# Kernel optimization log

Hardware: AMD Instinct MI355X
Metric: run time of the kernel (lower is better)

## Reference

```python
import jax, jax.numpy as jnp
import numpy as np


def Qmat(V):
    """Chain of Householder reflections: Q = I @ H(v_0) @ ... @ H(v_{d-1}).

    Faithful to the source: columns of V are normalized, H(v) = I - 2 v v^T.
    M @ H(v) == M - 2 (M v) v^T, so each step is a matvec + rank-1 update
    (same math as the source's full GEMM, O(d^2) per step instead of O(d^3)).
    """
    d = V.shape[0]
    # torch.norm(V.T, 2, dim=1) == L2 norm of each column of V
    norms = jnp.linalg.norm(V, axis=0)  # (d,)
    Vn = V / norms[None, :]

    def step(M, v):
        Mv = M @ v                        # (d,)
        return M - 2.0 * jnp.outer(Mv, v), None

    M0 = jnp.eye(d, dtype=V.dtype)
    M, _ = jax.lax.scan(step, M0, Vn.T)   # iterate over columns v_i
    return M


def setup_inputs() -> dict:
    key = jax.random.key(0)
    k1, k2 = jax.random.split(key)
    ci, co = 1024, 2048
    U = 0.05 * jax.random.normal(k1, (ci, ci), dtype=jnp.float32)
    V = 0.05 * jax.random.normal(k2, (co, co), dtype=jnp.float32)
    return {"U": U, "V": V}


def reference(U, V):
    ci, co = U.shape[0], V.shape[0]
    Qu = Qmat(U)  # (ci, ci) orthogonal
    Qv = Qmat(V)  # (co, co) orthogonal
    if ci < co:
        weight = Qu @ Qv[:ci, :]      # (ci, co)
    else:
        weight = Qu[:, :co] @ Qv      # (ci, co)
    return weight
```

## Files before the change

### kernel.cpp

```cpp
#include <hip/hip_runtime.h>
#include <hip/hip_bf16.h>
#include <cstdint>

#define CI 1024
#define CO 2048
#define LP 36

typedef float  fx4  __attribute__((ext_vector_type(4)));
typedef short  s16x4 __attribute__((ext_vector_type(4)));
typedef short  s16x8 __attribute__((ext_vector_type(8)));
typedef unsigned short u16;

#define MFMA(a,b,c) __builtin_amdgcn_mfma_f32_16x16x32_bf16((a),(b),(c),0,0,0)

__device__ __forceinline__ u16 f2b(float x) {
    __hip_bfloat16 h = __float2bfloat16(x);
    return __builtin_bit_cast(u16, h);
}
__device__ __forceinline__ float b2f(u16 u) {
    __hip_bfloat16 h = __builtin_bit_cast(__hip_bfloat16, u);
    return __bfloat162float(h);
}


__global__ __launch_bounds__(256) void colnorm2(const float* __restrict__ M, float* __restrict__ n2, int d) {
    int c = blockIdx.x * 256 + threadIdx.x;
    int r0 = blockIdx.y * 64;
    float s = 0.0f;
    for (int r = r0; r < r0 + 64; ++r) {
        float v = M[(size_t)r * d + c];
        s = fmaf(v, v, s);
    }
    atomicAdd(&n2[c], s);
}

__global__ __launch_bounds__(256) void trans_planes_n(const float* __restrict__ X, int d,
                                                      const float* __restrict__ n2,
                                                      u16* __restrict__ Th, u16* __restrict__ Tl) {
    __shared__ float tile[32][33];
    int t = threadIdx.x;
    int r = t >> 3, c4 = (t & 7) * 4;
    int bx = blockIdx.x, by = blockIdx.y;
    fx4 v = *(const fx4*)(X + (size_t)(by * 32 + r) * d + bx * 32 + c4);
    tile[r][c4 + 0] = v[0]; tile[r][c4 + 1] = v[1]; tile[r][c4 + 2] = v[2]; tile[r][c4 + 3] = v[3];
    __syncthreads();
    int a = bx * 32 + r;
    float sc = 1.0f / sqrtf(n2[a]);
    u16 h[4], l[4];
    #pragma unroll
    for (int j = 0; j < 4; ++j) {
        float f = tile[c4 + j][r] * sc;
        u16 hb = f2b(f);
        h[j] = hb;
        l[j] = f2b(f - b2f(hb));
    }
    size_t o = (size_t)a * d + by * 32 + c4;
    *(s16x4*)&Th[o] = *(s16x4*)&h[0];
    *(s16x4*)&Tl[o] = *(s16x4*)&l[0];
}

__global__ __launch_bounds__(256) void planes_n(const float* __restrict__ X, int d,
                                                const float* __restrict__ n2,
                                                u16* __restrict__ Ph, u16* __restrict__ Pl) {
    size_t idx = ((size_t)blockIdx.x * 256 + threadIdx.x) * 8;
    int c = (int)(idx & (size_t)(d - 1));
    fx4 v0 = *(const fx4*)(X + idx);
    fx4 v1 = *(const fx4*)(X + idx + 4);
    u16 h[8], l[8];
    #pragma unroll
    for (int j = 0; j < 8; ++j) {
        float f = ((j < 4) ? v0[j] : v1[j - 4]) * (1.0f / sqrtf(n2[c + j]));
        u16 hb = f2b(f);
        h[j] = hb;
        l[j] = f2b(f - b2f(hb));
    }
    *(s16x4*)&Ph[idx]     = *(s16x4*)&h[0];
    *(s16x4*)&Ph[idx + 4] = *(s16x4*)&h[4];
    *(s16x4*)&Pl[idx]     = *(s16x4*)&l[0];
    *(s16x4*)&Pl[idx + 4] = *(s16x4*)&l[4];
}

__global__ __launch_bounds__(256) void planes_conv(const float* __restrict__ X,
                                                   u16* __restrict__ Ph, u16* __restrict__ Pl) {
    size_t idx = ((size_t)blockIdx.x * 256 + threadIdx.x) * 8;
    fx4 v0 = *(const fx4*)(X + idx);
    fx4 v1 = *(const fx4*)(X + idx + 4);
    u16 h[8], l[8];
    #pragma unroll
    for (int j = 0; j < 8; ++j) {
        float f = (j < 4) ? v0[j] : v1[j - 4];
        u16 hb = f2b(f);
        h[j] = hb;
        l[j] = f2b(f - b2f(hb));
    }
    *(s16x4*)&Ph[idx]     = *(s16x4*)&h[0];
    *(s16x4*)&Ph[idx + 4] = *(s16x4*)&h[4];
    *(s16x4*)&Pl[idx]     = *(s16x4*)&l[0];
    *(s16x4*)&Pl[idx + 4] = *(s16x4*)&l[4];
}

__device__ __forceinline__ void mma_step(const u16 Ah[][LP], const u16 Al[][LP],
                                         const u16 Bh[][LP], const u16 Bl[][LP],
                                         int wr, int wc, int lane, fx4 acc[2][2]) {
    int kb = (lane >> 4) * 8;
    int rl = lane & 15;
    s16x8 ah[2], al[2], bh[2], bl[2];
    #pragma unroll
    for (int f = 0; f < 2; ++f) {
        int ra = wr * 32 + f * 16 + rl;
        s16x4 p = *(const s16x4*)&Ah[ra][kb];
        s16x4 q = *(const s16x4*)&Ah[ra][kb + 4];
        ah[f] = __builtin_shufflevector(p, q, 0,1,2,3,4,5,6,7);
        p = *(const s16x4*)&Al[ra][kb];
        q = *(const s16x4*)&Al[ra][kb + 4];
        al[f] = __builtin_shufflevector(p, q, 0,1,2,3,4,5,6,7);
        int rb = wc * 32 + f * 16 + rl;
        p = *(const s16x4*)&Bh[rb][kb];
        q = *(const s16x4*)&Bh[rb][kb + 4];
        bh[f] = __builtin_shufflevector(p, q, 0,1,2,3,4,5,6,7);
        p = *(const s16x4*)&Bl[rb][kb];
        q = *(const s16x4*)&Bl[rb][kb + 4];
        bl[f] = __builtin_shufflevector(p, q, 0,1,2,3,4,5,6,7);
    }
    #pragma unroll
    for (int i = 0; i < 2; ++i)
        #pragma unroll
        for (int j = 0; j < 2; ++j) {
            acc[i][j] = MFMA(ah[i], bh[j], acc[i][j]);
            acc[i][j] = MFMA(ah[i], bl[j], acc[i][j]);
            acc[i][j] = MFMA(al[i], bh[j], acc[i][j]);
        }
}

__device__ __forceinline__ void stage_f32(const float* __restrict__ A, int ldA,
                                          int m0, int k0, int t, u16 Dh[][LP], u16 Dl[][LP]) {
    int row = t >> 2, kc = (t & 3) * 8;
    const float* p = A + (size_t)(m0 + row) * ldA + k0 + kc;
    fx4 v0 = *(const fx4*)p;
    fx4 v1 = *(const fx4*)(p + 4);
    u16 h[8], l[8];
    #pragma unroll
    for (int j = 0; j < 8; ++j) {
        float f = (j < 4) ? v0[j] : v1[j - 4];
        u16 hb = f2b(f);
        h[j] = hb;
        l[j] = f2b(f - b2f(hb));
    }
    *(s16x4*)&Dh[row][kc]     = *(s16x4*)&h[0];
    *(s16x4*)&Dh[row][kc + 4] = *(s16x4*)&h[4];
    *(s16x4*)&Dl[row][kc]     = *(s16x4*)&l[0];
    *(s16x4*)&Dl[row][kc + 4] = *(s16x4*)&l[4];
}

__device__ __forceinline__ void stage_planes(const u16* __restrict__ Ph, const u16* __restrict__ Pl, int ld,
                                             int n0, int k0, int t, u16 Dh[][LP], u16 Dl[][LP]) {
    int row = t >> 2, kc = (t & 3) * 8;
    size_t o = (size_t)(n0 + row) * ld + k0 + kc;
    *(s16x4*)&Dh[row][kc]     = *(const s16x4*)(Ph + o);
    *(s16x4*)&Dh[row][kc + 4] = *(const s16x4*)(Ph + o + 4);
    *(s16x4*)&Dl[row][kc]     = *(const s16x4*)(Pl + o);
    *(s16x4*)&Dl[row][kc + 4] = *(const s16x4*)(Pl + o + 4);
}

struct GJob {
    const u16* Ph; const u16* Pl; int ld;
    int a, b;
    float* out; int ldO;
};

__device__ __forceinline__ GJob gdecode(int t,
                                        const u16* Uh, const u16* Ul, const u16* Vh, const u16* Vl,
                                        float* Sd, float* Nt64, float* Nt128, float* Nt256, float* Nt512) {
    GJob g;
    if (t < 48) {
        bool isU = t < 16; int off = 64 * (isU ? t : t - 16);
        g.Ph = isU ? Uh : Vh; g.Pl = isU ? Ul : Vl; g.ld = isU ? CI : CO;
        g.a = off; g.b = off;
        g.out = Sd + (size_t)t * 4096; g.ldO = 64;
    } else if (t < 72) {
        int j = t - 48; bool isU = j < 8; int p = isU ? j : j - 8;
        int c0 = 128 * p, r1 = c0 + 64;
        g.Ph = isU ? Uh : Vh; g.Pl = isU ? Ul : Vl; g.ld = isU ? CI : CO;
        g.a = r1; g.b = c0;
        g.out = Nt64 + (size_t)j * 4096; g.ldO = 64;
    } else if (t < 120) {
        int j = t - 72; int pair = j >> 2, q = j & 3, my = q >> 1, mx = q & 1;
        bool isU = pair < 4; int p = isU ? pair : pair - 4;
        int c0 = 256 * p, r1 = c0 + 128;
        g.Ph = isU ? Uh : Vh; g.Pl = isU ? Ul : Vl; g.ld = isU ? CI : CO;
        g.a = r1 + 64 * my; g.b = c0 + 64 * mx;
        g.out = Nt128 + (size_t)pair * 16384 + (size_t)(64 * my) * 128 + 64 * mx; g.ldO = 128;
    } else if (t < 216) {
        int j = t - 120; int pair = j >> 4, q = j & 15, my = q >> 2, mx = q & 3;
        bool isU = pair < 2; int p = isU ? pair : pair - 2;
        int c0 = 512 * p, r1 = c0 + 256;
        g.Ph = isU ? Uh : Vh; g.Pl = isU ? Ul : Vl; g.ld = isU ? CI : CO;
        g.a = r1 + 64 * my; g.b = c0 + 64 * mx;
        g.out = Nt256 + (size_t)pair * 65536 + (size_t)(64 * my) * 256 + 64 * mx; g.ldO = 256;
    } else {
        int j = t - 216; int pair = j >> 6, q = j & 63, my = q >> 3, mx = q & 7;
        int c0 = 1024 * pair, r1 = c0 + 512;
        g.Ph = Vh; g.Pl = Vl; g.ld = CO;
        g.a = r1 + 64 * my; g.b = c0 + 64 * mx;
        g.out = Nt512 + (size_t)pair * 262144 + (size_t)(64 * my) * 512 + 64 * mx; g.ldO = 512;
    }
    return g;
}

__global__ __launch_bounds__(256) void gram_nt_sk(const u16* __restrict__ Uh, const u16* __restrict__ Ul,
                                                  const u16* __restrict__ Vh, const u16* __restrict__ Vl,
                                                  float* Sd, float* Nt64, float* Nt128, float* Nt256, float* Nt512,
                                                  float* __restrict__ Gp) {
    int tt = blockIdx.x, ks = blockIdx.y;
    GJob g = gdecode(tt, Uh, Ul, Vh, Vl, Sd, Nt64, Nt128, Nt256, Nt512);
    int kchunk = g.ld >> 3;
    int kb = ks * kchunk;
    float* C = Gp + ((size_t)tt * 8 + ks) * 4096;
    __shared__ u16 Ah[64][LP], Al[64][LP], Bh_[64][LP], Bl_[64][LP];
    int t = threadIdx.x, lane = t & 63, w = t >> 6, wr = w >> 1, wc = w & 1;
    fx4 acc[2][2] = {};
    for (int k0 = kb; k0 < kb + kchunk; k0 += 32) {
        stage_planes(g.Ph, g.Pl, g.ld, g.a, k0, t, Ah, Al);
        stage_planes(g.Ph, g.Pl, g.ld, g.b, k0, t, Bh_, Bl_);
        __syncthreads();
        mma_step(Ah, Al, Bh_, Bl_, wr, wc, lane, acc);
        __syncthreads();
    }
    #pragma unroll
    for (int fr = 0; fr < 2; ++fr)
        #pragma unroll
        for (int fc = 0; fc < 2; ++fc) {
            int row = wr * 32 + fr * 16 + ((lane >> 4) << 2);
            int col = wc * 32 + fc * 16 + (lane & 15);
            #pragma unroll
            for (int r = 0; r < 4; ++r)
                C[(size_t)(row + r) * 64 + col] = acc[fr][fc][r];
        }
}

__global__ __launch_bounds__(256) void gcombine(const float* __restrict__ Gp,
                                                const u16* Uh, const u16* Ul, const u16* Vh, const u16* Vl,
                                                float* Sd, float* Nt64, float* Nt128, float* Nt256, float* Nt512) {
    int tt = blockIdx.x;
    GJob g = gdecode(tt, Uh, Ul, Vh, Vl, Sd, Nt64, Nt128, Nt256, Nt512);
    const float* base = Gp + (size_t)tt * 8 * 4096;
    for (int i = threadIdx.x; i < 4096; i += 256) {
        float s = 0.0f;
        #pragma unroll
        for (int ks = 0; ks < 8; ++ks) s += base[(size_t)ks * 4096 + i];
        g.out[(size_t)(i >> 6) * g.ldO + (i & 63)] = s;
    }
}

__global__ __launch_bounds__(64) void diag_inv64(const float* __restrict__ Sd,
                                                 float* __restrict__ Ttu, float* __restrict__ Ttv) {
    int j = blockIdx.x;
    int y = blockIdx.y;
    const float* S = Sd + (size_t)y * 4096;
    float* T; int ldT, off;
    if (y < 16) { T = Ttu; ldT = CI; off = 64 * y; }
    else        { T = Ttv; ldT = CO; off = 64 * (y - 16); }
    float* Trow = T + (size_t)(off + j) * ldT + off;
    int l = threadIdx.x;
    float x = (l == j) ? 2.0f : 0.0f;
    float a = 0.0f;
    int jpad = (j + 7) & ~7;
    float q0=0,q1=0,q2=0,q3=0,q4=0,q5=0,q6=0,q7=0;
#define LR(Q, R) { int _r = (R); if (_r >= 1 && _r <= j) Q = S[(size_t)_r * 64 + l]; }
    LR(q0, jpad - 0) LR(q1, jpad - 1) LR(q2, jpad - 2) LR(q3, jpad - 3)
    LR(q4, jpad - 4) LR(q5, jpad - 5) LR(q6, jpad - 6) LR(q7, jpad - 7)
#define ST(Q) { \
    float yk = __shfl(x, k); \
    a = fmaf(Q, yk, a); \
    if (k <= j && l == k - 1) x = -2.0f * a; \
    int pr = k - 8; \
    if (pr >= 1) Q = S[(size_t)pr * 64 + l]; \
    --k; }
    int k = jpad;
    int ng = jpad >> 3;
    for (int g = 0; g < ng; ++g) {
        ST(q0) ST(q1) ST(q2) ST(q3) ST(q4) ST(q5) ST(q6) ST(q7)
    }
#undef ST
#undef LR
    Trow[l] = x;
}

__global__ __launch_bounds__(256) void merge64_fused(const float* __restrict__ Nt64,
                                                     float* __restrict__ Ttu, float* __restrict__ Ttv) {
    int p = blockIdx.x;
    bool isU = p < 8;
    float* Tt = isU ? Ttu : Ttv;
    int ldT = isU ? CI : CO;
    int pp = isU ? p : p - 8;
    int c0 = 128 * pp, r1 = c0 + 64;
    __shared__ float A[64][65], B[64][65], Tm[64][65];
    int t = threadIdx.x;
    int r = t >> 2, c = (t & 3) * 16;
    #pragma unroll
    for (int j = 0; j < 16; ++j) A[r][c + j] = Nt64[(size_t)p * 4096 + (size_t)r * 64 + c + j];
    #pragma unroll
    for (int j = 0; j < 16; ++j) B[r][c + j] = Tt[(size_t)(c0 + r) * ldT + c0 + c + j];
    __syncthreads();
    float acc[16];
    #pragma unroll
    for (int j = 0; j < 16; ++j) acc[j] = 0.0f;
    for (int k = 0; k < 64; ++k) {
        float av = A[r][k];
        #pragma unroll
        for (int j = 0; j < 16; ++j) acc[j] = fmaf(av, B[k][c + j], acc[j]);
    }
    __syncthreads();
    #pragma unroll
    for (int j = 0; j < 16; ++j) Tm[r][c + j] = acc[j];
    #pragma unroll
    for (int j = 0; j < 16; ++j) A[r][c + j] = Tt[(size_t)(r1 + r) * ldT + r1 + c + j];
    __syncthreads();
    #pragma unroll
    for (int j = 0; j < 16; ++j) acc[j] = 0.0f;
    for (int k = 0; k < 64; ++k) {
        float av = A[r][k];
        #pragma unroll
        for (int j = 0; j < 16; ++j) acc[j] = fmaf(av, Tm[k][c + j], acc[j]);
    }
    #pragma unroll
    for (int j = 0; j < 16; ++j)
        Tt[(size_t)(r1 + r) * ldT + c0 + c + j] = -acc[j];
}

__device__ __forceinline__ void fgemm_sk_body(const float* __restrict__ A, int lda,
                                              const float* __restrict__ B, int ldb,
                                              float* __restrict__ P, int kb, int klen) {
    int m0 = blockIdx.y * 64, n0 = blockIdx.x * 64;
    __shared__ float As[16][64];
    __shared__ float Bs[16][64];
    int tid = threadIdx.x;
    int tm = (tid >> 4) * 8, tn = (tid & 15) * 4;
    int ar = tid >> 2, ac = (tid & 3) * 4;
    int bk = tid >> 4, bn = (tid & 15) * 4;
    float acc[8][4] = {};
    for (int k0 = kb; k0 < kb + klen; k0 += 16) {
        #pragma unroll
        for (int p = 0; p < 2; ++p) {
            int r = ar + p * 32;
            fx4 av = *(const fx4*)(A + (size_t)(m0 + r) * lda + k0 + ac);
            As[ac + 0][r] = av[0]; As[ac + 1][r] = av[1]; As[ac + 2][r] = av[2]; As[ac + 3][r] = av[3];
        }
        #pragma unroll
        for (int p = 0; p < 2; ++p) {
            int kk = bk + p * 8;
            *(fx4*)&Bs[kk][bn] = *(const fx4*)(B + (size_t)(k0 + kk) * ldb + n0 + bn);
        }
        __syncthreads();
        #pragma unroll
        for (int k = 0; k < 16; ++k) {
            fx4 alo = *(const fx4*)&As[k][tm];
            fx4 ahi = *(const fx4*)&As[k][tm + 4];
            fx4 bv  = *(const fx4*)&Bs[k][tn];
            float aa[8] = {alo[0], alo[1], alo[2], alo[3], ahi[0], ahi[1], ahi[2], ahi[3]};
            float bb[4] = {bv[0], bv[1], bv[2], bv[3]};
            #pragma unroll
            for (int i = 0; i < 8; ++i)
                #pragma unroll
                for (int jj = 0; jj < 4; ++jj) acc[i][jj] = fmaf(aa[i], bb[jj], acc[i][jj]);
        }
        __syncthreads();
    }
    #pragma unroll
    for (int i = 0; i < 8; ++i) {
        fx4 v = { acc[i][0], acc[i][1], acc[i][2], acc[i][3] };
        *(fx4*)(P + (size_t)(tm + i) * 64 + tn) = v;
    }
}

__global__ __launch_bounds__(128) void merge_a_sk(const float* __restrict__ NtL, int s, int KS,
                                                  const float* __restrict__ Ttu, const float* __restrict__ Ttv,
                                                  int npu, float* __restrict__ Mp) {
    int z = blockIdx.z;
    int pair = z / KS, ks = z % KS;
    const float* Tt; int ldT, p;
    if (pair < npu) { Tt = Ttu; ldT = CI; p = pair; } else { Tt = Ttv; ldT = CO; p = pair - npu; }
    int c0 = 2 * s * p;
    int gx = s >> 6;
    int tile = (pair * gx + blockIdx.y) * gx + blockIdx.x;
    int klen = s / KS;
    fgemm_sk_body(NtL + (size_t)pair * s * s, s, Tt + (size_t)c0 * ldT + c0, ldT,
                  Mp + ((size_t)tile * KS + ks) * 4096, ks * klen, klen);
}

__global__ __launch_bounds__(128) void merge_b_sk(const float* __restrict__ tmp, int s, int KS,
                                                  const float* __restrict__ Ttu, const float* __restrict__ Ttv,
                                                  int npu, float* __restrict__ Mp) {
    int z = blockIdx.z;
    int pair = z / KS, ks = z % KS;
    const float* Tt; int ldT, p;
    if (pair < npu) { Tt = Ttu; ldT = CI; p = pair; } else { Tt = Ttv; ldT = CO; p = pair - npu; }
    int c0 = 2 * s * p, r1 = c0 + s;
    int gx = s >> 6;
    int tile = (pair * gx + blockIdx.y) * gx + blockIdx.x;
    int klen = s / KS;
    fgemm_sk_body(Tt + (size_t)r1 * ldT + r1, ldT, tmp + (size_t)pair * s * s, s,
                  Mp + ((size_t)tile * KS + ks) * 4096, ks * klen, klen);
}

__global__ __launch_bounds__(256) void macomb(const float* __restrict__ Mp, int KS, int s,
                                              float* __restrict__ tmp) {
    int tile = blockIdx.x;
    int gx = s >> 6, per = gx * gx;
    int pair = tile / per, rem = tile % per, by = rem / gx, bx = rem % gx;
    float* dst = tmp + (size_t)pair * s * s + (size_t)(by * 64) * s + bx * 64;
    const float* base = Mp + (size_t)tile * KS * 4096;
    for (int i = threadIdx.x; i < 4096; i += 256) {
        float v = 0.0f;
        for (int k = 0; k < KS; ++k) v += base[(size_t)k * 4096 + i];
        dst[(size_t)(i >> 6) * s + (i & 63)] = v;
    }
}

__global__ __launch_bounds__(256) void mbcomb(const float* __restrict__ Mp, int KS, int s, int npu,
                                              float* __restrict__ Ttu, float* __restrict__ Ttv) {
    int tile = blockIdx.x;
    int gx = s >> 6, per = gx * gx;
    int pair = tile / per, rem = tile % per, by = rem / gx, bx = rem % gx;
    float* Tt; int ldT, p;
    if (pair < npu) { Tt = Ttu; ldT = CI; p = pair; } else { Tt = Ttv; ldT = CO; p = pair - npu; }
    int c0 = 2 * s * p, r1 = c0 + s;
    float* dst = Tt + (size_t)(r1 + by * 64) * ldT + c0 + bx * 64;
    const float* base = Mp + (size_t)tile * KS * 4096;
    for (int i = threadIdx.x; i < 4096; i += 256) {
        float v = 0.0f;
        for (int k = 0; k < KS; ++k) v += base[(size_t)k * 4096 + i];
        dst[(size_t)(i >> 6) * ldT + (i & 63)] = -v;
    }
}

__global__ __launch_bounds__(256) void gemm_pp_sk(const u16* __restrict__ Ah_, const u16* __restrict__ Al_, int ldA,
                                                  const u16* __restrict__ Bh0, const u16* __restrict__ Bl0, int ldB,
                                                  float* __restrict__ Pp, int kchunk) {
    int N = gridDim.x * 64;
    size_t MN = (size_t)gridDim.x * gridDim.y * 4096;
    float* C = Pp + (size_t)blockIdx.z * MN;
    int kb = blockIdx.z * kchunk;
    __shared__ u16 Ah[64][LP], Al[64][LP], Bh_[64][LP], Bl_[64][LP];
    int t = threadIdx.x, lane = t & 63, w = t >> 6, wr = w >> 1, wc = w & 1;
    int m0 = blockIdx.y * 64, n0 = blockIdx.x * 64;
    fx4 acc[2][2] = {};
    for (int k0 = kb; k0 < kb + kchunk; k0 += 32) {
        stage_planes(Ah_, Al_, ldA, m0, k0, t, Ah, Al);
        stage_planes(Bh0, Bl0, ldB, n0, k0, t, Bh_, Bl_);
        __syncthreads();
        mma_step(Ah, Al, Bh_, Bl_, wr, wc, lane, acc);
        __syncthreads();
    }
    #pragma unroll
    for (int fr = 0; fr < 2; ++fr)
        #pragma unroll
        for (int fc = 0; fc < 2; ++fc) {
            int row = m0 + wr * 32 + fr * 16 + ((lane >> 4) << 2);
            int col = n0 + wc * 32 + fc * 16 + (lane & 15);
            #pragma unroll
            for (int r = 0; r < 4; ++r)
                C[(size_t)(row + r) * N + col] = acc[fr][fc][r];
        }
}

__global__ __launch_bounds__(256) void gemm_fp_sk(const float* __restrict__ A, int ldA,
                                                  const u16* __restrict__ Bh0, const u16* __restrict__ Bl0, int ldB,
                                                  float* __restrict__ Pp, int kchunk) {
    int N = gridDim.x * 64;
    size_t MN = (size_t)gridDim.x * gridDim.y * 4096;
    float* C = Pp + (size_t)blockIdx.z * MN;
    int kb = blockIdx.z * kchunk;
    __shared__ u16 Ah[64][LP], Al[64][LP], Bh_[64][LP], Bl_[64][LP];
    int t = threadIdx.x, lane = t & 63, w = t >> 6, wr = w >> 1, wc = w & 1;
    int m0 = blockIdx.y * 64, n0 = blockIdx.x * 64;
    fx4 acc[2][2] = {};
    for (int k0 = kb; k0 < kb + kchunk; k0 += 32) {
        stage_f32(A, ldA, m0, k0, t, Ah, Al);
        stage_planes(Bh0, Bl0, ldB, n0, k0, t, Bh_, Bl_);
        __syncthreads();
        mma_step(Ah, Al, Bh_, Bl_, wr, wc, lane, acc);
        __syncthreads();
    }
    #pragma unroll
    for (int fr = 0; fr < 2; ++fr)
        #pragma unroll
        for (int fc = 0; fc < 2; ++fc) {
            int row = m0 + wr * 32 + fr * 16 + ((lane >> 4) << 2);
            int col = n0 + wc * 32 + fc * 16 + (lane & 15);
            #pragma unroll
            for (int r = 0; r < 4; ++r)
                C[(size_t)(row + r) * N + col] = acc[fr][fc][r];
        }
}

template<int MODE>
__global__ __launch_bounds__(256) void combine(const float* __restrict__ Pp, int S,
                                               const float* __restrict__ aux, int ldaux,
                                               float* __restrict__ C, int N) {
    size_t MN = (size_t)gridDim.x * 2048;
    int gid = blockIdx.x * 256 + threadIdx.x;
    size_t idx = (size_t)gid * 8;
    int nv = N >> 3;
    int row = gid / nv, col = (gid % nv) * 8;
    fx4 s0 = *(const fx4*)(Pp + idx);
    fx4 s1 = *(const fx4*)(Pp + idx + 4);
    for (int s = 1; s < S; ++s) {
        const float* p = Pp + (size_t)s * MN + idx;
        s0 += *(const fx4*)p;
        s1 += *(const fx4*)(p + 4);
    }
    float out[8];
    #pragma unroll
    for (int j = 0; j < 8; ++j) {
        float a = (j < 4) ? s0[j] : s1[j - 4];
        if (MODE == 0)      out[j] = a;
        else if (MODE == 1) out[j] = ((col + j) == row ? 1.0f : 0.0f) - a;
        else if (MODE == 2) out[j] = aux[(size_t)row * ldaux + col + j] - a;
        else if (MODE == 3) out[j] = C[(size_t)row * N + col + j] - a;
        else                out[j] = ((col + j) < CI ? aux[(size_t)row * ldaux + col + j] : 0.0f) - a;
    }
    *(fx4*)(C + (size_t)row * N + col)     = *(fx4*)&out[0];
    *(fx4*)(C + (size_t)row * N + col + 4) = *(fx4*)&out[4];
}

extern "C" void kernel_launch(void* const* d_in, const int* in_sizes, int n_in,
                              void* d_out, int out_size, void* d_ws, size_t ws_size,
                              hipStream_t stream) {
    const float* U = (const float*)d_in[0];
    const float* V = (const float*)d_in[1];
    float* W = (float*)d_out;

    char* ws = (char*)d_ws;
    u16*   Unth = (u16*)  (ws + ((size_t)0   << 20));
    u16*   Untl = (u16*)  (ws + ((size_t)2   << 20));
    u16*   Unh  = (u16*)  (ws + ((size_t)4   << 20));
    u16*   Unl  = (u16*)  (ws + ((size_t)6   << 20));
    u16*   Vnth = (u16*)  (ws + ((size_t)8   << 20));
    u16*   Vntl = (u16*)  (ws + ((size_t)16  << 20));
    u16*   Vnh  = (u16*)  (ws + ((size_t)24  << 20));
    u16*   Vnl  = (u16*)  (ws + ((size_t)32  << 20));
    float* Ttu  = (float*)(ws + ((size_t)40  << 20));
    float* Ttv  = (float*)(ws + ((size_t)44  << 20));
    u16*   Mtuh = (u16*)  (ws + ((size_t)60  << 20));
    u16*   Mtul = (u16*)  (ws + ((size_t)62  << 20));
    u16*   Mtvh = (u16*)  (ws + ((size_t)64  << 20));
    u16*   Mtvl = (u16*)  (ws + ((size_t)72  << 20));
    float* Sd   = (float*)(ws + ((size_t)80  << 20));
    float* NtA  = (float*)(ws + ((size_t)81  << 20));
    float* tmp  = (float*)(ws + ((size_t)86  << 20));
    float* X1   = (float*)(ws + ((size_t)88  << 20));
    float* Qp   = (float*)(ws + ((size_t)90  << 20));
    float* H1u  = (float*)(ws + ((size_t)94  << 20));
    float* H2u  = (float*)(ws + ((size_t)96  << 20));
    float* Qu   = (float*)(ws + ((size_t)98  << 20));
    float* H1   = (float*)(ws + ((size_t)102 << 20));
    float* H2   = (float*)(ws + ((size_t)106 << 20));
    float* H3   = (float*)(ws + ((size_t)110 << 20));
    float* H4   = (float*)(ws + ((size_t)114 << 20));
    float* n2u  = (float*)(ws + ((size_t)118 << 20));
    float* n2v  = n2u + CI;
    float* Pp   = (float*)(ws + ((size_t)120 << 20));
    float* Gp   = (float*)(ws + ((size_t)120 << 20));
    float* Mp   = Gp;

    float* Nt64  = NtA;
    float* Nt128 = NtA + 98304;
    float* Nt256 = NtA + 294912;
    float* Nt512 = NtA + 688128;

    hipMemsetAsync(n2u, 0, (CI + CO) * sizeof(float), stream);
    colnorm2<<<dim3(CI / 256, CI / 64), dim3(256), 0, stream>>>(U, n2u, CI);
    colnorm2<<<dim3(CO / 256, CO / 64), dim3(256), 0, stream>>>(V, n2v, CO);

    trans_planes_n<<<dim3(CI / 32, CI / 32), dim3(256), 0, stream>>>(U, CI, n2u, Unth, Untl);
    trans_planes_n<<<dim3(CO / 32, CO / 32), dim3(256), 0, stream>>>(V, CO, n2v, Vnth, Vntl);
    planes_n<<<dim3(CI * CI / 2048), dim3(256), 0, stream>>>(U, CI, n2u, Unh, Unl);
    planes_n<<<dim3(CO * CO / 2048), dim3(256), 0, stream>>>(V, CO, n2v, Vnh, Vnl);

    gram_nt_sk<<<dim3(344, 8), dim3(256), 0, stream>>>(Unth, Untl, Vnth, Vntl,
                                                       Sd, Nt64, Nt128, Nt256, Nt512, Gp);
    gcombine<<<dim3(344), dim3(256), 0, stream>>>(Gp, Unth, Untl, Vnth, Vntl,
                                                  Sd, Nt64, Nt128, Nt256, Nt512);

    hipMemsetAsync(Ttu, 0, (size_t)20 << 20, stream);
    diag_inv64<<<dim3(64, 48), dim3(64), 0, stream>>>(Sd, Ttu, Ttv);
    merge64_fused<<<dim3(24), dim3(256), 0, stream>>>(Nt64, Ttu, Ttv);
    merge_a_sk<<<dim3(2, 2, 48), dim3(128), 0, stream>>>(Nt128, 128, 4, Ttu, Ttv, 4, Mp);
    macomb<<<dim3(48), dim3(256), 0, stream>>>(Mp, 4, 128, tmp);
    merge_b_sk<<<dim3(2, 2, 48), dim3(128), 0, stream>>>(tmp, 128, 4, Ttu, Ttv, 4, Mp);
    mbcomb<<<dim3(48), dim3(256), 0, stream>>>(Mp, 4, 128, 4, Ttu, Ttv);
    merge_a_sk<<<dim3(4, 4, 24), dim3(128), 0, stream>>>(Nt256, 256, 4, Ttu, Ttv, 2, Mp);
    macomb<<<dim3(96), dim3(256), 0, stream>>>(Mp, 4, 256, tmp);
    merge_b_sk<<<dim3(4, 4, 24), dim3(128), 0, stream>>>(tmp, 256, 4, Ttu, Ttv, 2, Mp);
    mbcomb<<<dim3(96), dim3(256), 0, stream>>>(Mp, 4, 256, 2, Ttu, Ttv);
    merge_a_sk<<<dim3(8, 8, 16), dim3(128), 0, stream>>>(Nt512, 512, 8, Ttu, Ttv, 0, Mp);
    macomb<<<dim3(128), dim3(256), 0, stream>>>(Mp, 8, 512, tmp);
    merge_b_sk<<<dim3(8, 8, 16), dim3(128), 0, stream>>>(tmp, 512, 8, Ttu, Ttv, 0, Mp);
    mbcomb<<<dim3(128), dim3(256), 0, stream>>>(Mp, 8, 512, 0, Ttu, Ttv);

    planes_conv<<<dim3(CI * CI / 2048), dim3(256), 0, stream>>>(Ttu, Mtuh, Mtul);
    planes_conv<<<dim3(CO * CO / 2048), dim3(256), 0, stream>>>(Ttv, Mtvh, Mtvl);

    gemm_pp_sk<<<dim3(8, 16, 4), dim3(256), 0, stream>>>(Unh, Unl, CI, Mtuh, Mtul, CI, Pp, 128);
    combine<0><<<dim3(CI * 512 / 2048), dim3(256), 0, stream>>>(Pp, 4, nullptr, 0, X1, 512);
    gemm_fp_sk<<<dim3(16, 16, 4), dim3(256), 0, stream>>>(X1, 512, Unh, Unl, CI, Pp, 128);
    combine<1><<<dim3(CI * CI / 2048), dim3(256), 0, stream>>>(Pp, 4, nullptr, 0, Qp, CI);
    gemm_fp_sk<<<dim3(8, 16, 4), dim3(256), 0, stream>>>(Qp, CI, Unth + (size_t)512 * CI, Untl + (size_t)512 * CI, CI, Pp, 256);
    combine<0><<<dim3(CI * 512 / 2048), dim3(256), 0, stream>>>(Pp, 4, nullptr, 0, H1u, 512);
    gemm_fp_sk<<<dim3(8, 16, 4), dim3(256), 0, stream>>>(H1u, 512, Mtuh + (size_t)512 * CI + 512,
                                                         Mtul + (size_t)512 * CI + 512, CI, Pp, 128);
    combine<0><<<dim3(CI * 512 / 2048), dim3(256), 0, stream>>>(Pp, 4, nullptr, 0, H2u, 512);
    gemm_fp_sk<<<dim3(16, 16, 4), dim3(256), 0, stream>>>(H2u, 512, Unh + 512, Unl + 512, CI, Pp, 128);
    combine<2><<<dim3(CI * CI / 2048), dim3(256), 0, stream>>>(Pp, 4, Qp, CI, Qu, CI);

    gemm_fp_sk<<<dim3(16, 16, 4), dim3(256), 0, stream>>>(Qu, CI, Vnth, Vntl, CO, Pp, 256);
    combine<0><<<dim3(CI * CI / 2048), dim3(256), 0, stream>>>(Pp, 4, nullptr, 0, H1, CI);
    gemm_fp_sk<<<dim3(16, 16, 4), dim3(256), 0, stream>>>(H1, CI, Mtvh, Mtvl, CO, Pp, 256);
    combine<0><<<dim3(CI * CI / 2048), dim3(256), 0, stream>>>(Pp, 4, nullptr, 0, H2, CI);
    gemm_fp_sk<<<dim3(32, 16, 2), dim3(256), 0, stream>>>(H2, CI, Vnh, Vnl, CO, Pp, 512);
    combine<4><<<dim3(CI * CO / 2048), dim3(256), 0, stream>>>(Pp, 2, Qu, CI, W, CO);
    gemm_fp_sk<<<dim3(16, 16, 4), dim3(256), 0, stream>>>(W, CO, Vnth + (size_t)1024 * CO, Vntl + (size_t)1024 * CO, CO, Pp, 512);
    combine<0><<<dim3(CI * CI / 2048), dim3(256), 0, stream>>>(Pp, 4, nullptr, 0, H3, CI);
    gemm_fp_sk<<<dim3(16, 16, 4), dim3(256), 0, stream>>>(H3, CI, Mtvh + (size_t)1024 * CO + 1024,
                                                          Mtvl + (size_t)1024 * CO + 1024, CO, Pp, 256);
    combine<0><<<dim3(CI * CI / 2048), dim3(256), 0, stream>>>(Pp, 4, nullptr, 0, H4, CI);
    gemm_fp_sk<<<dim3(32, 16, 2), dim3(256), 0, stream>>>(H4, CI, Vnh + 1024, Vnl + 1024, CO, Pp, 512);
    combine<3><<<dim3(CI * CO / 2048), dim3(256), 0, stream>>>(Pp, 2, nullptr, 0, W, CO);
}
```

Before: 504.9 us.

## Double-buffer LDS tiles with register prefetch in the split-K GEMM kernels

Three split-K GEMM kernels (gram, plane-plane, f32-plane) now load the next k-tile into registers while MFMAs run on the current LDS buffer, then commit it to the other half of a double-buffered shared array. This removes one __syncthreads per iteration and hides global load latency behind compute. For diagonal Gram tiles (a==b) the B tile is not loaded again and A is reused as B. The cost is twice the LDS footprint and more registers, which may lower occupancy.

```diff
diff --git a/kernel.cpp b/kernel.cpp
--- a/kernel.cpp
+++ b/kernel.cpp
@@ -132,34 +132,48 @@
         }
 }
 
-__device__ __forceinline__ void stage_f32(const float* __restrict__ A, int ldA,
-                                          int m0, int k0, int t, u16 Dh[][LP], u16 Dl[][LP]) {
+struct PF { s16x4 a, b, c, d; };
+__device__ __forceinline__ PF fetch_pl(const u16* __restrict__ Ph, const u16* __restrict__ Pl, int ld,
+                                       int n0, int k0, int t) {
+    int row = t >> 2, kc = (t & 3) * 8;
+    size_t o = (size_t)(n0 + row) * ld + k0 + kc;
+    PF f;
+    f.a = *(const s16x4*)(Ph + o);
+    f.b = *(const s16x4*)(Ph + o + 4);
+    f.c = *(const s16x4*)(Pl + o);
+    f.d = *(const s16x4*)(Pl + o + 4);
+    return f;
+}
+__device__ __forceinline__ void commit_pl(const PF& f, u16 Dh[][LP], u16 Dl[][LP], int t) {
+    int row = t >> 2, kc = (t & 3) * 8;
+    *(s16x4*)&Dh[row][kc]     = f.a;
+    *(s16x4*)&Dh[row][kc + 4] = f.b;
+    *(s16x4*)&Dl[row][kc]     = f.c;
+    *(s16x4*)&Dl[row][kc + 4] = f.d;
+}
+struct FF { fx4 v0, v1; };
+__device__ __forceinline__ FF fetch_f32(const float* __restrict__ A, int ldA, int m0, int k0, int t) {
     int row = t >> 2, kc = (t & 3) * 8;
     const float* p = A + (size_t)(m0 + row) * ldA + k0 + kc;
-    fx4 v0 = *(const fx4*)p;
-    fx4 v1 = *(const fx4*)(p + 4);
+    FF f;
+    f.v0 = *(const fx4*)p;
+    f.v1 = *(const fx4*)(p + 4);
+    return f;
+}
+__device__ __forceinline__ void commit_f32(const FF& f, u16 Dh[][LP], u16 Dl[][LP], int t) {
+    int row = t >> 2, kc = (t & 3) * 8;
     u16 h[8], l[8];
     #pragma unroll
     for (int j = 0; j < 8; ++j) {
-        float f = (j < 4) ? v0[j] : v1[j - 4];
-        u16 hb = f2b(f);
+        float v = (j < 4) ? f.v0[j] : f.v1[j - 4];
+        u16 hb = f2b(v);
         h[j] = hb;
-        l[j] = f2b(f - b2f(hb));
+        l[j] = f2b(v - b2f(hb));
     }
     *(s16x4*)&Dh[row][kc]     = *(s16x4*)&h[0];
     *(s16x4*)&Dh[row][kc + 4] = *(s16x4*)&h[4];
     *(s16x4*)&Dl[row][kc]     = *(s16x4*)&l[0];
     *(s16x4*)&Dl[row][kc + 4] = *(s16x4*)&l[4];
-}
-
-__device__ __forceinline__ void stage_planes(const u16* __restrict__ Ph, const u16* __restrict__ Pl, int ld,
-                                             int n0, int k0, int t, u16 Dh[][LP], u16 Dl[][LP]) {
-    int row = t >> 2, kc = (t & 3) * 8;
-    size_t o = (size_t)(n0 + row) * ld + k0 + kc;
-    *(s16x4*)&Dh[row][kc]     = *(const s16x4*)(Ph + o);
-    *(s16x4*)&Dh[row][kc + 4] = *(const s16x4*)(Ph + o + 4);
-    *(s16x4*)&Dl[row][kc]     = *(const s16x4*)(Pl + o);
-    *(s16x4*)&Dl[row][kc + 4] = *(const s16x4*)(Pl + o + 4);
 }
 
 struct GJob {
@@ -213,18 +227,34 @@
                                                   float* __restrict__ Gp) {
     int tt = blockIdx.x, ks = blockIdx.y;
     GJob g = gdecode(tt, Uh, Ul, Vh, Vl, Sd, Nt64, Nt128, Nt256, Nt512);
+    bool same = (g.a == g.b);
     int kchunk = g.ld >> 3;
     int kb = ks * kchunk;
     float* C = Gp + ((size_t)tt * 8 + ks) * 4096;
-    __shared__ u16 Ah[64][LP], Al[64][LP], Bh_[64][LP], Bl_[64][LP];
+    __shared__ u16 Ah[2][64][LP], Al[2][64][LP], Bh_[2][64][LP], Bl_[2][64][LP];
     int t = threadIdx.x, lane = t & 63, w = t >> 6, wr = w >> 1, wc = w & 1;
     fx4 acc[2][2] = {};
-    for (int k0 = kb; k0 < kb + kchunk; k0 += 32) {
-        stage_planes(g.Ph, g.Pl, g.ld, g.a, k0, t, Ah, Al);
-        stage_planes(g.Ph, g.Pl, g.ld, g.b, k0, t, Bh_, Bl_);
-        __syncthreads();
-        mma_step(Ah, Al, Bh_, Bl_, wr, wc, lane, acc);
-        __syncthreads();
+    PF fa = fetch_pl(g.Ph, g.Pl, g.ld, g.a, kb, t);
+    PF fb;
+    if (!same) fb = fetch_pl(g.Ph, g.Pl, g.ld, g.b, kb, t);
+    commit_pl(fa, Ah[0], Al[0], t);
+    if (!same) commit_pl(fb, Bh_[0], Bl_[0], t);
+    __syncthreads();
+    int nt = kchunk >> 5;
+    for (int it = 0; it < nt; ++it) {
+        int cur = it & 1;
+        if (it + 1 < nt) {
+            int k0 = kb + (it + 1) * 32;
+            fa = fetch_pl(g.Ph, g.Pl, g.ld, g.a, k0, t);
+            if (!same) fb = fetch_pl(g.Ph, g.Pl, g.ld, g.b, k0, t);
+        }
+        mma_step(Ah[cur], Al[cur], same ? Ah[cur] : Bh_[cur], same ? Al[cur] : Bl_[cur], wr, wc, lane, acc);
+        if (it + 1 < nt) {
+            int nx = cur ^ 1;
+            commit_pl(fa, Ah[nx], Al[nx], t);
+            if (!same) commit_pl(fb, Bh_[nx], Bl_[nx], t);
+            __syncthreads();
+        }
     }
     #pragma unroll
     for (int fr = 0; fr < 2; ++fr)
@@ -441,16 +471,30 @@
     size_t MN = (size_t)gridDim.x * gridDim.y * 4096;
     float* C = Pp + (size_t)blockIdx.z * MN;
     int kb = blockIdx.z * kchunk;
-    __shared__ u16 Ah[64][LP], Al[64][LP], Bh_[64][LP], Bl_[64][LP];
+    __shared__ u16 Ah[2][64][LP], Al[2][64][LP], Bh_[2][64][LP], Bl_[2][64][LP];
     int t = threadIdx.x, lane = t & 63, w = t >> 6, wr = w >> 1, wc = w & 1;
     int m0 = blockIdx.y * 64, n0 = blockIdx.x * 64;
     fx4 acc[2][2] = {};
-    for (int k0 = kb; k0 < kb + kchunk; k0 += 32) {
-        stage_planes(Ah_, Al_, ldA, m0, k0, t, Ah, Al);
-        stage_planes(Bh0, Bl0, ldB, n0, k0, t, Bh_, Bl_);
-        __syncthreads();
-        mma_step(Ah, Al, Bh_, Bl_, wr, wc, lane, acc);
-        __syncthreads();
+    PF fa = fetch_pl(Ah_, Al_, ldA, m0, kb, t);
+    PF fb = fetch_pl(Bh0, Bl0, ldB, n0, kb, t);
+    commit_pl(fa, Ah[0], Al[0], t);
+    commit_pl(fb, Bh_[0], Bl_[0], t);
+    __syncthreads();
+    int nt = kchunk >> 5;
+    for (int it = 0; it < nt; ++it) {
+        int cur = it & 1;
+        if (it + 1 < nt) {
+            int k0 = kb + (it + 1) * 32;
+            fa = fetch_pl(Ah_, Al_, ldA, m0, k0, t);
+            fb = fetch_pl(Bh0, Bl0, ldB, n0, k0, t);
+        }
+        mma_step(Ah[cur], Al[cur], Bh_[cur], Bl_[cur], wr, wc, lane, acc);
+        if (it + 1 < nt) {
+            int nx = cur ^ 1;
+            commit_pl(fa, Ah[nx], Al[nx], t);
+            commit_pl(fb, Bh_[nx], Bl_[nx], t);
+            __syncthreads();
+        }
     }
     #pragma unroll
     for (int fr = 0; fr < 2; ++fr)
@@ -471,16 +515,30 @@
     size_t MN = (size_t)gridDim.x * gridDim.y * 4096;
     float* C = Pp + (size_t)blockIdx.z * MN;
     int kb = blockIdx.z * kchunk;
-    __shared__ u16 Ah[64][LP], Al[64][LP], Bh_[64][LP], Bl_[64][LP];
+    __shared__ u16 Ah[2][64][LP], Al[2][64][LP], Bh_[2][64][LP], Bl_[2][64][LP];
     int t = threadIdx.x, lane = t & 63, w = t >> 6, wr = w >> 1, wc = w & 1;
     int m0 = blockIdx.y * 64, n0 = blockIdx.x * 64;
     fx4 acc[2][2] = {};
-    for (int k0 = kb; k0 < kb + kchunk; k0 += 32) {
-        stage_f32(A, ldA, m0, k0, t, Ah, Al);
-        stage_planes(Bh0, Bl0, ldB, n0, k0, t, Bh_, Bl_);
-        __syncthreads();
-        mma_step(Ah, Al, Bh_, Bl_, wr, wc, lane, acc);
-        __syncthreads();
+    FF fa = fetch_f32(A, ldA, m0, kb, t);
+    PF fb = fetch_pl(Bh0, Bl0, ldB, n0, kb, t);
+    commit_f32(fa, Ah[0], Al[0], t);
+    commit_pl(fb, Bh_[0], Bl_[0], t);
+    __syncthreads();
+    int nt = kchunk >> 5;
+    for (int it = 0; it < nt; ++it) {
+        int cur = it & 1;
+        if (it + 1 < nt) {
+            int k0 = kb + (it + 1) * 32;
+            fa = fetch_f32(A, ldA, m0, k0, t);
+            fb = fetch_pl(Bh0, Bl0, ldB, n0, k0, t);
+        }
+        mma_step(Ah[cur], Al[cur], Bh_[cur], Bl_[cur], wr, wc, lane, acc);
+        if (it + 1 < nt) {
+            int nx = cur ^ 1;
+            commit_f32(fa, Ah[nx], Al[nx], t);
+            commit_pl(fb, Bh_[nx], Bl_[nx], t);
+            __syncthreads();
+        }
     }
     #pragma unroll
     for (int fr = 0; fr < 2; ++fr)
```

Result: no change. 500.3 us (median of 2 runs) (-0.9%).

## Emit bf16 hi/lo planes from combine and prefetch GEMM tiles into registers

Applied to the files above, without the earlier changes.

The combine kernels now write bf16 hi/lo split planes directly, and fp32 only where a later step still needs it. That lets every downstream GEMM use the plane-input kernel instead of re-splitting fp32 operands inside each tile load, and it removes the fp32 intermediate buffers. The GEMM and Gram loops now prefetch the next k-tile into registers while the MFMAs run on the current shared-memory tile. The Gram kernel also skips loading B when it is identical to A. The LDS row pitch grows to 40 so that 16-byte vector LDS loads stay aligned, at the cost of slightly more shared memory and extra register pressure from the prefetch.

```diff
diff --git a/kernel.cpp b/kernel.cpp
--- a/kernel.cpp
+++ b/kernel.cpp
@@ -4,7 +4,7 @@
 
 #define CI 1024
 #define CO 2048
-#define LP 36
+#define LP 40
 
 typedef float  fx4  __attribute__((ext_vector_type(4)));
 typedef short  s16x4 __attribute__((ext_vector_type(4)));
@@ -108,19 +108,11 @@
     #pragma unroll
     for (int f = 0; f < 2; ++f) {
         int ra = wr * 32 + f * 16 + rl;
-        s16x4 p = *(const s16x4*)&Ah[ra][kb];
-        s16x4 q = *(const s16x4*)&Ah[ra][kb + 4];
-        ah[f] = __builtin_shufflevector(p, q, 0,1,2,3,4,5,6,7);
-        p = *(const s16x4*)&Al[ra][kb];
-        q = *(const s16x4*)&Al[ra][kb + 4];
-        al[f] = __builtin_shufflevector(p, q, 0,1,2,3,4,5,6,7);
+        ah[f] = *(const s16x8*)&Ah[ra][kb];
+        al[f] = *(const s16x8*)&Al[ra][kb];
         int rb = wc * 32 + f * 16 + rl;
-        p = *(const s16x4*)&Bh[rb][kb];
-        q = *(const s16x4*)&Bh[rb][kb + 4];
-        bh[f] = __builtin_shufflevector(p, q, 0,1,2,3,4,5,6,7);
-        p = *(const s16x4*)&Bl[rb][kb];
-        q = *(const s16x4*)&Bl[rb][kb + 4];
-        bl[f] = __builtin_shufflevector(p, q, 0,1,2,3,4,5,6,7);
+        bh[f] = *(const s16x8*)&Bh[rb][kb];
+        bl[f] = *(const s16x8*)&Bl[rb][kb];
     }
     #pragma unroll
     for (int i = 0; i < 2; ++i)
@@ -132,34 +124,20 @@
         }
 }
 
-__device__ __forceinline__ void stage_f32(const float* __restrict__ A, int ldA,
-                                          int m0, int k0, int t, u16 Dh[][LP], u16 Dl[][LP]) {
-    int row = t >> 2, kc = (t & 3) * 8;
-    const float* p = A + (size_t)(m0 + row) * ldA + k0 + kc;
-    fx4 v0 = *(const fx4*)p;
-    fx4 v1 = *(const fx4*)(p + 4);
-    u16 h[8], l[8];
-    #pragma unroll
-    for (int j = 0; j < 8; ++j) {
-        float f = (j < 4) ? v0[j] : v1[j - 4];
-        u16 hb = f2b(f);
-        h[j] = hb;
-        l[j] = f2b(f - b2f(hb));
-    }
-    *(s16x4*)&Dh[row][kc]     = *(s16x4*)&h[0];
-    *(s16x4*)&Dh[row][kc + 4] = *(s16x4*)&h[4];
-    *(s16x4*)&Dl[row][kc]     = *(s16x4*)&l[0];
-    *(s16x4*)&Dl[row][kc + 4] = *(s16x4*)&l[4];
-}
-
-__device__ __forceinline__ void stage_planes(const u16* __restrict__ Ph, const u16* __restrict__ Pl, int ld,
-                                             int n0, int k0, int t, u16 Dh[][LP], u16 Dl[][LP]) {
+struct PF { s16x8 h, l; };
+__device__ __forceinline__ PF fetch_pl(const u16* __restrict__ Ph, const u16* __restrict__ Pl, int ld,
+                                       int n0, int k0, int t) {
     int row = t >> 2, kc = (t & 3) * 8;
     size_t o = (size_t)(n0 + row) * ld + k0 + kc;
-    *(s16x4*)&Dh[row][kc]     = *(const s16x4*)(Ph + o);
-    *(s16x4*)&Dh[row][kc + 4] = *(const s16x4*)(Ph + o + 4);
-    *(s16x4*)&Dl[row][kc]     = *(const s16x4*)(Pl + o);
-    *(s16x4*)&Dl[row][kc + 4] = *(const s16x4*)(Pl + o + 4);
+    PF f;
+    f.h = *(const s16x8*)(Ph + o);
+    f.l = *(const s16x8*)(Pl + o);
+    return f;
+}
+__device__ __forceinline__ void commit_pl(const PF& f, u16 Dh[][LP], u16 Dl[][LP], int t) {
+    int row = t >> 2, kc = (t & 3) * 8;
+    *(s16x8*)&Dh[row][kc] = f.h;
+    *(s16x8*)&Dl[row][kc] = f.l;
 }
 
 struct GJob {
@@ -213,17 +191,27 @@
                                                   float* __restrict__ Gp) {
     int tt = blockIdx.x, ks = blockIdx.y;
     GJob g = gdecode(tt, Uh, Ul, Vh, Vl, Sd, Nt64, Nt128, Nt256, Nt512);
+    bool same = (g.a == g.b);
     int kchunk = g.ld >> 3;
     int kb = ks * kchunk;
     float* C = Gp + ((size_t)tt * 8 + ks) * 4096;
     __shared__ u16 Ah[64][LP], Al[64][LP], Bh_[64][LP], Bl_[64][LP];
     int t = threadIdx.x, lane = t & 63, w = t >> 6, wr = w >> 1, wc = w & 1;
     fx4 acc[2][2] = {};
-    for (int k0 = kb; k0 < kb + kchunk; k0 += 32) {
-        stage_planes(g.Ph, g.Pl, g.ld, g.a, k0, t, Ah, Al);
-        stage_planes(g.Ph, g.Pl, g.ld, g.b, k0, t, Bh_, Bl_);
+    PF fa = fetch_pl(g.Ph, g.Pl, g.ld, g.a, kb, t);
+    PF fb;
+    if (!same) fb = fetch_pl(g.Ph, g.Pl, g.ld, g.b, kb, t);
+    int nt = kchunk >> 5;
+    for (int it = 0; it < nt; ++it) {
+        commit_pl(fa, Ah, Al, t);
+        if (!same) commit_pl(fb, Bh_, Bl_, t);
         __syncthreads();
-        mma_step(Ah, Al, Bh_, Bl_, wr, wc, lane, acc);
+        if (it + 1 < nt) {
+            int k0 = kb + (it + 1) * 32;
+            fa = fetch_pl(g.Ph, g.Pl, g.ld, g.a, k0, t);
+            if (!same) fb = fetch_pl(g.Ph, g.Pl, g.ld, g.b, k0, t);
+        }
+        mma_step(Ah, Al, same ? Ah : Bh_, same ? Al : Bl_, wr, wc, lane, acc);
         __syncthreads();
     }
     #pragma unroll
@@ -445,10 +433,18 @@
     int t = threadIdx.x, lane = t & 63, w = t >> 6, wr = w >> 1, wc = w & 1;
     int m0 = blockIdx.y * 64, n0 = blockIdx.x * 64;
     fx4 acc[2][2] = {};
-    for (int k0 = kb; k0 < kb + kchunk; k0 += 32) {
-        stage_planes(Ah_, Al_, ldA, m0, k0, t, Ah, Al);
-        stage_planes(Bh0, Bl0, ldB, n0, k0, t, Bh_, Bl_);
+    PF fa = fetch_pl(Ah_, Al_, ldA, m0, kb, t);
+    PF fb = fetch_pl(Bh0, Bl0, ldB, n0, kb, t);
+    int nt = kchunk >> 5;
+    for (int it = 0; it < nt; ++it) {
+        commit_pl(fa, Ah, Al, t);
+        commit_pl(fb, Bh_, Bl_, t);
         __syncthreads();
+        if (it + 1 < nt) {
+            int k0 = kb + (it + 1) * 32;
+            fa = fetch_pl(Ah_, Al_, ldA, m0, k0, t);
+            fb = fetch_pl(Bh0, Bl0, ldB, n0, k0, t);
+        }
         mma_step(Ah, Al, Bh_, Bl_, wr, wc, lane, acc);
         __syncthreads();
     }
@@ -464,40 +460,11 @@
         }
 }
 
-__global__ __launch_bounds__(256) void gemm_fp_sk(const float* __restrict__ A, int ldA,
-                                                  const u16* __restrict__ Bh0, const u16* __restrict__ Bl0, int ldB,
-                                                  float* __restrict__ Pp, int kchunk) {
-    int N = gridDim.x * 64;
-    size_t MN = (size_t)gridDim.x * gridDim.y * 4096;
-    float* C = Pp + (size_t)blockIdx.z * MN;
-    int kb = blockIdx.z * kchunk;
-    __shared__ u16 Ah[64][LP], Al[64][LP], Bh_[64][LP], Bl_[64][LP];
-    int t = threadIdx.x, lane = t & 63, w = t >> 6, wr = w >> 1, wc = w & 1;
-    int m0 = blockIdx.y * 64, n0 = blockIdx.x * 64;
-    fx4 acc[2][2] = {};
-    for (int k0 = kb; k0 < kb + kchunk; k0 += 32) {
-        stage_f32(A, ldA, m0, k0, t, Ah, Al);
-        stage_planes(Bh0, Bl0, ldB, n0, k0, t, Bh_, Bl_);
-        __syncthreads();
-        mma_step(Ah, Al, Bh_, Bl_, wr, wc, lane, acc);
-        __syncthreads();
-    }
-    #pragma unroll
-    for (int fr = 0; fr < 2; ++fr)
-        #pragma unroll
-        for (int fc = 0; fc < 2; ++fc) {
-            int row = m0 + wr * 32 + fr * 16 + ((lane >> 4) << 2);
-            int col = n0 + wc * 32 + fc * 16 + (lane & 15);
-            #pragma unroll
-            for (int r = 0; r < 4; ++r)
-                C[(size_t)(row + r) * N + col] = acc[fr][fc][r];
-        }
-}
-
-template<int MODE>
+template<int MODE, int OUT>
 __global__ __launch_bounds__(256) void combine(const float* __restrict__ Pp, int S,
                                                const float* __restrict__ aux, int ldaux,
-                                               float* __restrict__ C, int N) {
+                                               float* __restrict__ C,
+                                               u16* __restrict__ Ph, u16* __restrict__ Pl, int N) {
     size_t MN = (size_t)gridDim.x * 2048;
     int gid = blockIdx.x * 256 + threadIdx.x;
     size_t idx = (size_t)gid * 8;
@@ -520,8 +487,24 @@
         else if (MODE == 3) out[j] = C[(size_t)row * N + col + j] - a;
         else                out[j] = ((col + j) < CI ? aux[(size_t)row * ldaux + col + j] : 0.0f) - a;
     }
-    *(fx4*)(C + (size_t)row * N + col)     = *(fx4*)&out[0];
-    *(fx4*)(C + (size_t)row * N + col + 4) = *(fx4*)&out[4];
+    size_t o = (size_t)row * N + col;
+    if (OUT & 1) {
+        *(fx4*)(C + o)     = *(fx4*)&out[0];
+        *(fx4*)(C + o + 4) = *(fx4*)&out[4];
+    }
+    if (OUT & 2) {
+        u16 h[8], l[8];
+        #pragma unroll
+        for (int j = 0; j < 8; ++j) {
+            u16 hb = f2b(out[j]);
+            h[j] = hb;
+            l[j] = f2b(out[j] - b2f(hb));
+        }
+        *(s16x4*)&Ph[o]     = *(s16x4*)&h[0];
+        *(s16x4*)&Ph[o + 4] = *(s16x4*)&h[4];
+        *(s16x4*)&Pl[o]     = *(s16x4*)&l[0];
+        *(s16x4*)&Pl[o + 4] = *(s16x4*)&l[4];
+    }
 }
 
 extern "C" void kernel_launch(void* const* d_in, const int* in_sizes, int n_in,
@@ -549,20 +532,33 @@
     float* Sd   = (float*)(ws + ((size_t)80  << 20));
     float* NtA  = (float*)(ws + ((size_t)81  << 20));
     float* tmp  = (float*)(ws + ((size_t)86  << 20));
-    float* X1   = (float*)(ws + ((size_t)88  << 20));
     float* Qp   = (float*)(ws + ((size_t)90  << 20));
-    float* H1u  = (float*)(ws + ((size_t)94  << 20));
-    float* H2u  = (float*)(ws + ((size_t)96  << 20));
     float* Qu   = (float*)(ws + ((size_t)98  << 20));
-    float* H1   = (float*)(ws + ((size_t)102 << 20));
-    float* H2   = (float*)(ws + ((size_t)106 << 20));
-    float* H3   = (float*)(ws + ((size_t)110 << 20));
-    float* H4   = (float*)(ws + ((size_t)114 << 20));
     float* n2u  = (float*)(ws + ((size_t)118 << 20));
     float* n2v  = n2u + CI;
     float* Pp   = (float*)(ws + ((size_t)120 << 20));
     float* Gp   = (float*)(ws + ((size_t)120 << 20));
     float* Mp   = Gp;
+    u16* X1h  = (u16*)(ws + ((size_t)170 << 20));
+    u16* X1l  = (u16*)(ws + ((size_t)171 << 20));
+    u16* Qph  = (u16*)(ws + ((size_t)172 << 20));
+    u16* Qpl  = (u16*)(ws + ((size_t)174 << 20));
+    u16* H1uh = (u16*)(ws + ((size_t)176 << 20));
+    u16* H1ul = (u16*)(ws + ((size_t)177 << 20));
+    u16* H2uh = (u16*)(ws + ((size_t)178 << 20));
+    u16* H2ul = (u16*)(ws + ((size_t)179 << 20));
+    u16* Quh  = (u16*)(ws + ((size_t)180 << 20));
+    u16* Qul  = (u16*)(ws + ((size_t)182 << 20));
+    u16* H1h  = (u16*)(ws + ((size_t)184 << 20));
+    u16* H1l  = (u16*)(ws + ((size_t)186 << 20));
+    u16* H2h  = (u16*)(ws + ((size_t)188 << 20));
+    u16* H2l  = (u16*)(ws + ((size_t)190 << 20));
+    u16* Wh   = (u16*)(ws + ((size_t)192 << 20));
+    u16* Wl   = (u16*)(ws + ((size_t)196 << 20));
+    u16* H3h  = (u16*)(ws + ((size_t)200 << 20));
+    u16* H3l  = (u16*)(ws + ((size_t)202 << 20));
+    u16* H4h  = (u16*)(ws + ((size_t)204 << 20));
+    u16* H4l  = (u16*)(ws + ((size_t)206 << 20));
 
     float* Nt64  = NtA;
     float* Nt128 = NtA + 98304;
@@ -603,28 +599,28 @@
     planes_conv<<<dim3(CO * CO / 2048), dim3(256), 0, stream>>>(Ttv, Mtvh, Mtvl);
 
     gemm_pp_sk<<<dim3(8, 16, 4), dim3(256), 0, stream>>>(Unh, Unl, CI, Mtuh, Mtul, CI, Pp, 128);
-    combine<0><<<dim3(CI * 512 / 2048), dim3(256), 0, stream>>>(Pp, 4, nullptr, 0, X1, 512);
-    gemm_fp_sk<<<dim3(16, 16, 4), dim3(256), 0, stream>>>(X1, 512, Unh, Unl, CI, Pp, 128);
-    combine<1><<<dim3(CI * CI / 2048), dim3(256), 0, stream>>>(Pp, 4, nullptr, 0, Qp, CI);
-    gemm_fp_sk<<<dim3(8, 16, 4), dim3(256), 0, stream>>>(Qp, CI, Unth + (size_t)512 * CI, Untl + (size_t)512 * CI, CI, Pp, 256);
-    combine<0><<<dim3(CI * 512 / 2048), dim3(256), 0, stream>>>(Pp, 4, nullptr, 0, H1u, 512);
-    gemm_fp_sk<<<dim3(8, 16, 4), dim3(256), 0, stream>>>(H1u, 512, Mtuh + (size_t)512 * CI + 512,
+    combine<0, 2><<<dim3(CI * 512 / 2048), dim3(256), 0, stream>>>(Pp, 4, nullptr, 0, nullptr, X1h, X1l, 512);
+    gemm_pp_sk<<<dim3(16, 16, 4), dim3(256), 0, stream>>>(X1h, X1l, 512, Unh, Unl, CI, Pp, 128);
+    combine<1, 3><<<dim3(CI * CI / 2048), dim3(256), 0, stream>>>(Pp, 4, nullptr, 0, Qp, Qph, Qpl, CI);
+    gemm_pp_sk<<<dim3(8, 16, 4), dim3(256), 0, stream>>>(Qph, Qpl, CI, Unth + (size_t)512 * CI, Untl + (size_t)512 * CI, CI, Pp, 256);
+    combine<0, 2><<<dim3(CI * 512 / 2048), dim3(256), 0, stream>>>(Pp, 4, nullptr, 0, nullptr, H1uh, H1ul, 512);
+    gemm_pp_sk<<<dim3(8, 16, 4), dim3(256), 0, stream>>>(H1uh, H1ul, 512, Mtuh + (size_t)512 * CI + 512,
                                                          Mtul + (size_t)512 * CI + 512, CI, Pp, 128);
-    combine<0><<<dim3(CI * 512 / 2048), dim3(256), 0, stream>>>(Pp, 4, nullptr, 0, H2u, 512);
-    gemm_fp_sk<<<dim3(16, 16, 4), dim3(256), 0, stream>>>(H2u, 512, Unh + 512, Unl + 512, CI, Pp, 128);
-    combine<2><<<dim3(CI * CI / 2048), dim3(256), 0, stream>>>(Pp, 4, Qp, CI, Qu, CI);
-
-    gemm_fp_sk<<<dim3(16, 16, 4), dim3(256), 0, stream>>>(Qu, CI, Vnth, Vntl, CO, Pp, 256);
-    combine<0><<<dim3(CI * CI / 2048), dim3(256), 0, stream>>>(Pp, 4, nullptr, 0, H1, CI);
-    gemm_fp_sk<<<dim3(16, 16, 4), dim3(256), 0, stream>>>(H1, CI, Mtvh, Mtvl, CO, Pp, 256);
-    combine<0><<<dim3(CI * CI / 2048), dim3(256), 0, stream>>>(Pp, 4, nullptr, 0, H2, CI);
-    gemm_fp_sk<<<dim3(32, 16, 2), dim3(256), 0, stream>>>(H2, CI, Vnh, Vnl, CO, Pp, 512);
-    combine<4><<<dim3(CI * CO / 2048), dim3(256), 0, stream>>>(Pp, 2, Qu, CI, W, CO);
-    gemm_fp_sk<<<dim3(16, 16, 4), dim3(256), 0, stream>>>(W, CO, Vnth + (size_t)1024 * CO, Vntl + (size_t)1024 * CO, CO, Pp, 512);
-    combine<0><<<dim3(CI * CI / 2048), dim3(256), 0, stream>>>(Pp, 4, nullptr, 0, H3, CI);
-    gemm_fp_sk<<<dim3(16, 16, 4), dim3(256), 0, stream>>>(H3, CI, Mtvh + (size_t)1024 * CO + 1024,
+    combine<0, 2><<<dim3(CI * 512 / 2048), dim3(256), 0, stream>>>(Pp, 4, nullptr, 0, nullptr, H2uh, H2ul, 512);
+    gemm_pp_sk<<<dim3(16, 16, 4), dim3(256), 0, stream>>>(H2uh, H2ul, 512, Unh + 512, Unl + 512, CI, Pp, 128);
+    combine<2, 3><<<dim3(CI * CI / 2048), dim3(256), 0, stream>>>(Pp, 4, Qp, CI, Qu, Quh, Qul, CI);
+
+    gemm_pp_sk<<<dim3(16, 16, 4), dim3(256), 0, stream>>>(Quh, Qul, CI, Vnth, Vntl, CO, Pp, 256);
+    combine<0, 2><<<dim3(CI * CI / 2048), dim3(256), 0, stream>>>(Pp, 4, nullptr, 0, nullptr, H1h, H1l, CI);
+    gemm_pp_sk<<<dim3(16, 16, 4), dim3(256), 0, stream>>>(H1h, H1l, CI, Mtvh, Mtvl, CO, Pp, 256);
+    combine<0, 2><<<dim3(CI * CI / 2048), dim3(256), 0, stream>>>(Pp, 4, nullptr, 0, nullptr, H2h, H2l, CI);
+    gemm_pp_sk<<<dim3(32, 16, 2), dim3(256), 0, stream>>>(H2h, H2l, CI, Vnh, Vnl, CO, Pp, 512);
+    combine<4, 3><<<dim3(CI * CO / 2048), dim3(256), 0, stream>>>(Pp, 2, Qu, CI, W, Wh, Wl, CO);
+    gemm_pp_sk<<<dim3(16, 16, 4), dim3(256), 0, stream>>>(Wh, Wl, CO, Vnth + (size_t)1024 * CO, Vntl + (size_t)1024 * CO, CO, Pp, 512);
+    combine<0, 2><<<dim3(CI * CI / 2048), dim3(256), 0, stream>>>(Pp, 4, nullptr, 0, nullptr, H3h, H3l, CI);
+    gemm_pp_sk<<<dim3(16, 16, 4), dim3(256), 0, stream>>>(H3h, H3l, CI, Mtvh + (size_t)1024 * CO + 1024,
                                                           Mtvl + (size_t)1024 * CO + 1024, CO, Pp, 256);
-    combine<0><<<dim3(CI * CI / 2048), dim3(256), 0, stream>>>(Pp, 4, nullptr, 0, H4, CI);
-    gemm_fp_sk<<<dim3(32, 16, 2), dim3(256), 0, stream>>>(H4, CI, Vnh + 1024, Vnl + 1024, CO, Pp, 512);
-    combine<3><<<dim3(CI * CO / 2048), dim3(256), 0, stream>>>(Pp, 2, nullptr, 0, W, CO);
-}
+    combine<0, 2><<<dim3(CI * CI / 2048), dim3(256), 0, stream>>>(Pp, 4, nullptr, 0, nullptr, H4h, H4l, CI);
+    gemm_pp_sk<<<dim3(32, 16, 2), dim3(256), 0, stream>>>(H4h, H4l, CI, Vnh + 1024, Vnl + 1024, CO, Pp, 512);
+    combine<3, 1><<<dim3(CI * CO / 2048), dim3(256), 0, stream>>>(Pp, 2, nullptr, 0, W, nullptr, nullptr, CO);
+}
```

After: 513.3 us. Within noise of the previous version (+1.7%).
